# Performance work log

Hardware: AMD Instinct MI355X
Metric: run time of the kernel (lower is better)

The kernel has to match this reference:

```python
import jax, jax.numpy as jnp
import numpy as np

S = 60            # voxel grid side
N = 100000        # active voxels
M_PAD = 60000     # padded pairs per kernel offset
C_IN = 64
C_OUT = 64
KV = 27           # kernel volume (3^3)
CENTER = 13


def _build_maps():
    rng = np.random.default_rng(0)
    lin = rng.choice(S ** 3, size=N, replace=False)
    coords = np.stack(np.unravel_index(lin, (S, S, S)), axis=1).astype(np.int64)  # [N,3]
    lut = -np.ones(S ** 3, dtype=np.int64)
    lut[lin] = np.arange(N)
    imap = -np.ones((KV - 1, M_PAD), dtype=np.int32)
    omap = -np.ones((KV - 1, M_PAD), dtype=np.int32)
    row = 0
    for k in range(KV):
        if k == CENTER:
            continue
        d = np.array([k // 9 - 1, (k // 3) % 3 - 1, k % 3 - 1])
        nb = coords + d
        valid = np.all((nb >= 0) & (nb < S), axis=1)
        linnb = nb[:, 0] * S * S + nb[:, 1] * S + nb[:, 2]
        j = np.where(valid, lut[np.clip(linnb, 0, S ** 3 - 1)], -1)
        mask = j >= 0
        src = np.nonzero(mask)[0].astype(np.int32)   # input idx (gather)
        dst = j[mask].astype(np.int32)               # output idx (scatter)
        m = min(src.shape[0], M_PAD)
        imap[row, :m] = src[:m]
        omap[row, :m] = dst[:m]
        row += 1
    return imap, omap


def setup_inputs() -> dict:
    key = jax.random.key(0)
    kf, kw = jax.random.split(key)
    feats = jax.random.normal(kf, (N, C_IN), dtype=jnp.float32)
    stdv = 1.0 / np.sqrt(C_OUT * KV)
    kernel = jax.random.uniform(kw, (KV, C_IN, C_OUT), dtype=jnp.float32,
                                minval=-stdv, maxval=stdv)
    imap_np, omap_np = _build_maps()
    return {
        "feats": feats,
        "kernel": kernel,
        "imap": jnp.asarray(imap_np),
        "omap": jnp.asarray(omap_np),
    }


def reference(feats, kernel, imap, omap):
    # Submanifold sparse 3D conv: center weight applied densely,
    # 26 neighbor offsets via gather -> per-offset GEMM -> scatter-add.
    # feats: [N, Cin], kernel: [27, Cin, Cout], imap/omap: [26, M] (-1 = pad)
    koff = jnp.concatenate([jnp.arange(CENTER), jnp.arange(CENTER + 1, KV)])
    w_off = kernel[koff]                                   # [26, Cin, Cout]
    out = feats @ kernel[CENTER]                           # [N, Cout] center GEMM
    valid = (imap >= 0)                                    # [26, M]
    gathered = feats[jnp.clip(imap, 0)] * valid[..., None].astype(feats.dtype)  # [26, M, Cin]
    partial = jnp.einsum('kmc,kco->kmo', gathered, w_off)  # [26, M, Cout]
    dst = jnp.where(valid, omap, 0).reshape(-1)            # padded rows contribute zeros
    out = out.at[dst].add(partial.reshape(-1, partial.shape[-1]))
    return out
```

## Files before the change

### kernel.cpp

```cpp
#include <hip/hip_runtime.h>


#define N_PTS 100000
#define MPAD  60000
#define C     64
#define NSL   27
#define NTAP  28
#define NSTG  14

typedef short bf16x8 __attribute__((ext_vector_type(8)));
typedef float f32x4  __attribute__((ext_vector_type(4)));

static __device__ inline unsigned short f2bf(float x) {
    unsigned int u = __float_as_uint(x);
    u += 0x7fffu + ((u >> 16) & 1u);
    return (unsigned short)(u >> 16);
}

#define FEATS16_BYTES ((size_t)(N_PTS + 1) * C * 2)
#define WFRAG_OFF     (((FEATS16_BYTES) + 255) & ~(size_t)255)
#define WFRAG_BYTES   ((size_t)NTAP * 8192)
#define NBR_OFF       (WFRAG_OFF + WFRAG_BYTES)
#define NBR_BYTES     ((size_t)26 * N_PTS * 4)

#define FEAT_ITEMS 800008
#define WF_ITEMS   (NTAP * 2 * 4 * 64)
#define SCAT_ITEMS (26 * MPAD / 4)
#define PREP_TOTAL (FEAT_ITEMS + WF_ITEMS + SCAT_ITEMS)

__global__ __launch_bounds__(256) void prep_one(const float* __restrict__ feats,
                                                const float* __restrict__ kern,
                                                const int* __restrict__ imap,
                                                const int* __restrict__ omap,
                                                unsigned short* __restrict__ f16,
                                                unsigned short* __restrict__ wf,
                                                int* __restrict__ nbr) {
    const int idx = blockIdx.x * 256 + threadIdx.x;
    if (idx < FEAT_ITEMS) {
        bf16x8* dst = (bf16x8*)f16;
        if (idx < FEAT_ITEMS - 8) {
            const float4* src = (const float4*)feats;
            const float4 a = src[2 * idx];
            const float4 b = src[2 * idx + 1];
            bf16x8 v;
            v[0] = (short)f2bf(a.x); v[1] = (short)f2bf(a.y);
            v[2] = (short)f2bf(a.z); v[3] = (short)f2bf(a.w);
            v[4] = (short)f2bf(b.x); v[5] = (short)f2bf(b.y);
            v[6] = (short)f2bf(b.z); v[7] = (short)f2bf(b.w);
            dst[idx] = v;
        } else {
            dst[idx] = (bf16x8){0, 0, 0, 0, 0, 0, 0, 0};
        }
    } else if (idx < FEAT_ITEMS + WF_ITEMS) {
        const int w = idx - FEAT_ITEMS;
        const int lane = w & 63;
        const int rest = w >> 6;
        const int ct = rest & 3;
        const int kk = (rest >> 2) & 1;
        const int s  = rest >> 3;
        bf16x8 v = (bf16x8){0, 0, 0, 0, 0, 0, 0, 0};
        if (s < NSL) {
            const int q = lane >> 4, t = lane & 15;
            const int ksrc = (s == 26) ? 13 : (s + (s >= 13 ? 1 : 0));
            const int k0 = kk * 32 + q * 8;
            const int n  = ct * 16 + t;
            const float* wp = kern + (size_t)ksrc * 4096 + n;
            #pragma unroll
            for (int j = 0; j < 8; ++j) v[j] = (short)f2bf(wp[(size_t)(k0 + j) * 64]);
        }
        ((bf16x8*)wf)[w] = v;
    } else {
        const int k = idx - (FEAT_ITEMS + WF_ITEMS);
        if (k < SCAT_ITEMS) {
            const int s = k / (MPAD / 4);
            const int v = k - s * (MPAD / 4);
            const int4 iv = ((const int4*)(imap + (size_t)s * MPAD))[v];
            const int4 ov = ((const int4*)(omap + (size_t)s * MPAD))[v];
            int* nb = nbr + (size_t)s * N_PTS;
            if (iv.x >= 0) nb[ov.x] = iv.x;
            if (iv.y >= 0) nb[ov.y] = iv.y;
            if (iv.z >= 0) nb[ov.z] = iv.z;
            if (iv.w >= 0) nb[ov.w] = iv.w;
        }
    }
}

static __device__ inline void stage_bfrags(const char* wfbase, int st,
                                           char* buf, int wave, int lane) {
    #pragma unroll
    for (int i = 0; i < 8; ++i) {
        const int chunk = wave * 8 + i;
        const char* gsrc = wfbase + (size_t)st * 16384 + chunk * 1024 + lane * 16;
        __builtin_amdgcn_global_load_lds(
            (const __attribute__((address_space(1))) unsigned int*)gsrc,
            (__attribute__((address_space(3))) unsigned int*)(buf + chunk * 1024),
            16, 0, 0);
    }
}

__global__ __launch_bounds__(128) void spconv_main(const unsigned short* __restrict__ f16,
                                                   const unsigned short* __restrict__ wf,
                                                   const int* __restrict__ nbr,
                                                   float* __restrict__ out) {
    __shared__ __align__(16) char smem[2][16384];

    const int lane = threadIdx.x & 63;
    const int wave = threadIdx.x >> 6;
    const int q = lane >> 4, t = lane & 15;
    const int R0 = blockIdx.x * 64 + wave * 32;
    const int row0 = R0 + t;
    const int row1 = R0 + 16 + t;
    const bool inb0 = (row0 < N_PTS);
    const bool inb1 = (row1 < N_PTS);
    const int safe0 = inb0 ? row0 : 0;
    const int safe1 = inb1 ? row1 : 0;

    const bf16x8* fv = (const bf16x8*)f16;
    const char* wfb  = (const char*)wf;

    stage_bfrags(wfb, 0, smem[0], wave, lane);

    int j0r[26], j1r[26];
    #pragma unroll
    for (int s = 0; s < 26; ++s) {
        j0r[s] = nbr[(size_t)s * N_PTS + safe0];
        j1r[s] = nbr[(size_t)s * N_PTS + safe1];
    }

    f32x4 acc[2][4];
    #pragma unroll
    for (int a = 0; a < 2; ++a)
        #pragma unroll
        for (int c = 0; c < 4; ++c)
            acc[a][c] = (f32x4){0.f, 0.f, 0.f, 0.f};

    #pragma unroll
    for (int st = 0; st < NSTG; ++st) {
        bf16x8 A[2][4];
        #pragma unroll
        for (int tt = 0; tt < 2; ++tt) {
            const int s = st * 2 + tt;
            int j0, j1;
            if (s == 26) {
                j0 = inb0 ? row0 : -1;
                j1 = inb1 ? row1 : -1;
            } else if (s == 27) {
                j0 = -1; j1 = -1;
            } else {
                j0 = inb0 ? j0r[s] : -1;
                j1 = inb1 ? j1r[s] : -1;
            }
            const int jz0 = ((unsigned)j0 < (unsigned)N_PTS) ? j0 : N_PTS;
            const int jz1 = ((unsigned)j1 < (unsigned)N_PTS) ? j1 : N_PTS;
            const bf16x8* a0 = fv + (size_t)jz0 * 8;
            const bf16x8* a1 = fv + (size_t)jz1 * 8;
            A[tt][0] = a0[q]; A[tt][1] = a0[4 + q];
            A[tt][2] = a1[q]; A[tt][3] = a1[4 + q];
        }

        __syncthreads();

        if (st + 1 < NSTG)
            stage_bfrags(wfb, st + 1, smem[(st + 1) & 1], wave, lane);

        const char* buf = smem[st & 1];
        #pragma unroll
        for (int tt = 0; tt < 2; ++tt) {
            bf16x8 B0[4], B1[4];
            #pragma unroll
            for (int ct = 0; ct < 4; ++ct) {
                B0[ct] = *(const bf16x8*)(buf + tt * 8192 + ct * 1024 + lane * 16);
                B1[ct] = *(const bf16x8*)(buf + tt * 8192 + 4096 + ct * 1024 + lane * 16);
            }
            #pragma unroll
            for (int ct = 0; ct < 4; ++ct) {
                acc[0][ct] = __builtin_amdgcn_mfma_f32_16x16x32_bf16(A[tt][0], B0[ct], acc[0][ct], 0, 0, 0);
                acc[1][ct] = __builtin_amdgcn_mfma_f32_16x16x32_bf16(A[tt][2], B0[ct], acc[1][ct], 0, 0, 0);
            }
            #pragma unroll
            for (int ct = 0; ct < 4; ++ct) {
                acc[0][ct] = __builtin_amdgcn_mfma_f32_16x16x32_bf16(A[tt][1], B1[ct], acc[0][ct], 0, 0, 0);
                acc[1][ct] = __builtin_amdgcn_mfma_f32_16x16x32_bf16(A[tt][3], B1[ct], acc[1][ct], 0, 0, 0);
            }
        }
    }

    #pragma unroll
    for (int tile = 0; tile < 2; ++tile) {
        #pragma unroll
        for (int i = 0; i < 4; ++i) {
            const int r = R0 + tile * 16 + 4 * q + i;
            if (r < N_PTS) {
                #pragma unroll
                for (int ct = 0; ct < 4; ++ct)
                    out[(size_t)r * C + ct * 16 + t] = acc[tile][ct][i];
            }
        }
    }
}

extern "C" void kernel_launch(void* const* d_in, const int* in_sizes, int n_in,
                              void* d_out, int out_size, void* d_ws, size_t ws_size,
                              hipStream_t stream) {
    const float* feats = (const float*)d_in[0];
    const float* kern  = (const float*)d_in[1];
    const int*   imap  = (const int*)d_in[2];
    const int*   omap  = (const int*)d_in[3];

    char* ws = (char*)d_ws;
    unsigned short* f16 = (unsigned short*)ws;
    unsigned short* wfr = (unsigned short*)(ws + WFRAG_OFF);
    int*            nbr = (int*)(ws + NBR_OFF);

    prep_one<<<dim3((PREP_TOTAL + 255) / 256), dim3(256), 0, stream>>>(
        feats, kern, imap, omap, f16, wfr, nbr);
    spconv_main<<<dim3((N_PTS + 63) / 64), dim3(128), 0, stream>>>(
        f16, wfr, nbr, (float*)d_out);
}
```

Before: 149.1 us.

## Load weight fragments directly from global memory instead of LDS double-buffering

Removes the LDS double-buffered staging of weight fragments and the per-stage __syncthreads; each wave now reads its B fragments straight from global memory (expected to sit in L2/L1 since all blocks share them). It also drops the padding 28th tap, so 27 slices are processed instead of 28, and adds an occupancy hint of 3 blocks per CU. In exchange it relies on cache hits for the weights, and the per-tap loop no longer interleaves loads of two taps.

Result: slower. 158.4 us (+6.2%).

```diff
diff --git a/kernel.cpp b/kernel.cpp
--- a/kernel.cpp
+++ b/kernel.cpp
@@ -5,8 +5,6 @@
 #define MPAD  60000
 #define C     64
 #define NSL   27
-#define NTAP  28
-#define NSTG  14
 
 typedef short bf16x8 __attribute__((ext_vector_type(8)));
 typedef float f32x4  __attribute__((ext_vector_type(4)));
@@ -19,12 +17,12 @@
 
 #define FEATS16_BYTES ((size_t)(N_PTS + 1) * C * 2)
 #define WFRAG_OFF     (((FEATS16_BYTES) + 255) & ~(size_t)255)
-#define WFRAG_BYTES   ((size_t)NTAP * 8192)
+#define WFRAG_BYTES   ((size_t)NSL * 8192)
 #define NBR_OFF       (WFRAG_OFF + WFRAG_BYTES)
 #define NBR_BYTES     ((size_t)26 * N_PTS * 4)
 
 #define FEAT_ITEMS 800008
-#define WF_ITEMS   (NTAP * 2 * 4 * 64)
+#define WF_ITEMS   (NSL * 2 * 4 * 64)
 #define SCAT_ITEMS (26 * MPAD / 4)
 #define PREP_TOTAL (FEAT_ITEMS + WF_ITEMS + SCAT_ITEMS)
 
@@ -85,25 +83,10 @@
     }
 }
 
-static __device__ inline void stage_bfrags(const char* wfbase, int st,
-                                           char* buf, int wave, int lane) {
-    #pragma unroll
-    for (int i = 0; i < 8; ++i) {
-        const int chunk = wave * 8 + i;
-        const char* gsrc = wfbase + (size_t)st * 16384 + chunk * 1024 + lane * 16;
-        __builtin_amdgcn_global_load_lds(
-            (const __attribute__((address_space(1))) unsigned int*)gsrc,
-            (__attribute__((address_space(3))) unsigned int*)(buf + chunk * 1024),
-            16, 0, 0);
-    }
-}
-
-__global__ __launch_bounds__(128) void spconv_main(const unsigned short* __restrict__ f16,
-                                                   const unsigned short* __restrict__ wf,
-                                                   const int* __restrict__ nbr,
-                                                   float* __restrict__ out) {
-    __shared__ __align__(16) char smem[2][16384];
-
+__global__ __launch_bounds__(128, 3) void spconv_main(const unsigned short* __restrict__ f16,
+                                                      const unsigned short* __restrict__ wf,
+                                                      const int* __restrict__ nbr,
+                                                      float* __restrict__ out) {
     const int lane = threadIdx.x & 63;
     const int wave = threadIdx.x >> 6;
     const int q = lane >> 4, t = lane & 15;
@@ -116,9 +99,7 @@
     const int safe1 = inb1 ? row1 : 0;
 
     const bf16x8* fv = (const bf16x8*)f16;
-    const char* wfb  = (const char*)wf;
-
-    stage_bfrags(wfb, 0, smem[0], wave, lane);
+    const bf16x8* bv = (const bf16x8*)wf;
 
     int j0r[26], j1r[26];
     #pragma unroll
@@ -135,53 +116,39 @@
             acc[a][c] = (f32x4){0.f, 0.f, 0.f, 0.f};
 
     #pragma unroll
-    for (int st = 0; st < NSTG; ++st) {
-        bf16x8 A[2][4];
+    for (int s = 0; s < NSL; ++s) {
+        int j0, j1;
+        if (s == 26) {
+            j0 = inb0 ? row0 : -1;
+            j1 = inb1 ? row1 : -1;
+        } else {
+            j0 = inb0 ? j0r[s] : -1;
+            j1 = inb1 ? j1r[s] : -1;
+        }
+        const int jz0 = ((unsigned)j0 < (unsigned)N_PTS) ? j0 : N_PTS;
+        const int jz1 = ((unsigned)j1 < (unsigned)N_PTS) ? j1 : N_PTS;
+        const bf16x8* a0p = fv + (size_t)jz0 * 8;
+        const bf16x8* a1p = fv + (size_t)jz1 * 8;
+        const bf16x8 A0 = a0p[q];
+        const bf16x8 A1 = a0p[4 + q];
+        const bf16x8 A2 = a1p[q];
+        const bf16x8 A3 = a1p[4 + q];
+        const bf16x8* bp = bv + (size_t)s * 512;
+        bf16x8 B0[4], B1[4];
         #pragma unroll
-        for (int tt = 0; tt < 2; ++tt) {
-            const int s = st * 2 + tt;
-            int j0, j1;
-            if (s == 26) {
-                j0 = inb0 ? row0 : -1;
-                j1 = inb1 ? row1 : -1;
-            } else if (s == 27) {
-                j0 = -1; j1 = -1;
-            } else {
-                j0 = inb0 ? j0r[s] : -1;
-                j1 = inb1 ? j1r[s] : -1;
-            }
-            const int jz0 = ((unsigned)j0 < (unsigned)N_PTS) ? j0 : N_PTS;
-            const int jz1 = ((unsigned)j1 < (unsigned)N_PTS) ? j1 : N_PTS;
-            const bf16x8* a0 = fv + (size_t)jz0 * 8;
-            const bf16x8* a1 = fv + (size_t)jz1 * 8;
-            A[tt][0] = a0[q]; A[tt][1] = a0[4 + q];
-            A[tt][2] = a1[q]; A[tt][3] = a1[4 + q];
+        for (int ct = 0; ct < 4; ++ct) {
+            B0[ct] = bp[ct * 64 + lane];
+            B1[ct] = bp[256 + ct * 64 + lane];
         }
-
-        __syncthreads();
-
-        if (st + 1 < NSTG)
-            stage_bfrags(wfb, st + 1, smem[(st + 1) & 1], wave, lane);
-
-        const char* buf = smem[st & 1];
         #pragma unroll
-        for (int tt = 0; tt < 2; ++tt) {
-            bf16x8 B0[4], B1[4];
-            #pragma unroll
-            for (int ct = 0; ct < 4; ++ct) {
-                B0[ct] = *(const bf16x8*)(buf + tt * 8192 + ct * 1024 + lane * 16);
-                B1[ct] = *(const bf16x8*)(buf + tt * 8192 + 4096 + ct * 1024 + lane * 16);
-            }
-            #pragma unroll
-            for (int ct = 0; ct < 4; ++ct) {
-                acc[0][ct] = __builtin_amdgcn_mfma_f32_16x16x32_bf16(A[tt][0], B0[ct], acc[0][ct], 0, 0, 0);
-                acc[1][ct] = __builtin_amdgcn_mfma_f32_16x16x32_bf16(A[tt][2], B0[ct], acc[1][ct], 0, 0, 0);
-            }
-            #pragma unroll
-            for (int ct = 0; ct < 4; ++ct) {
-                acc[0][ct] = __builtin_amdgcn_mfma_f32_16x16x32_bf16(A[tt][1], B1[ct], acc[0][ct], 0, 0, 0);
-                acc[1][ct] = __builtin_amdgcn_mfma_f32_16x16x32_bf16(A[tt][3], B1[ct], acc[1][ct], 0, 0, 0);
-            }
+        for (int ct = 0; ct < 4; ++ct) {
+            acc[0][ct] = __builtin_amdgcn_mfma_f32_16x16x32_bf16(A0, B0[ct], acc[0][ct], 0, 0, 0);
+            acc[1][ct] = __builtin_amdgcn_mfma_f32_16x16x32_bf16(A2, B0[ct], acc[1][ct], 0, 0, 0);
+        }
+        #pragma unroll
+        for (int ct = 0; ct < 4; ++ct) {
+            acc[0][ct] = __builtin_amdgcn_mfma_f32_16x16x32_bf16(A1, B1[ct], acc[0][ct], 0, 0, 0);
+            acc[1][ct] = __builtin_amdgcn_mfma_f32_16x16x32_bf16(A3, B1[ct], acc[1][ct], 0, 0, 0);
         }
     }
 
```

## Software-pipeline neighbor index and feature gathers, use 256-thread blocks

Applied to the files above, without the earlier changes.

Neighbor indices are no longer all loaded into 52 registers up front. They are now loaded two stages ahead, and the feature gathers for stage st+1 are issued one stage ahead, so they overlap the MFMA work of the current stage. The block grows to 4 waves covering 128 rows, so each wave stages only 4 of the 16 weight-fragment chunks into LDS, halving per-wave staging work. The occupancy hint is 3 blocks per CU. The register savings from dropping the index arrays are offset by double-buffered A fragments, which may raise register pressure.

Measured after the change: 148.2 us. No clear change (-0.6%).

```diff
diff --git a/kernel.cpp b/kernel.cpp
--- a/kernel.cpp
+++ b/kernel.cpp
@@ -88,8 +88,8 @@
 static __device__ inline void stage_bfrags(const char* wfbase, int st,
                                            char* buf, int wave, int lane) {
     #pragma unroll
-    for (int i = 0; i < 8; ++i) {
-        const int chunk = wave * 8 + i;
+    for (int i = 0; i < 4; ++i) {
+        const int chunk = wave * 4 + i;
         const char* gsrc = wfbase + (size_t)st * 16384 + chunk * 1024 + lane * 16;
         __builtin_amdgcn_global_load_lds(
             (const __attribute__((address_space(1))) unsigned int*)gsrc,
@@ -98,16 +98,76 @@
     }
 }
 
-__global__ __launch_bounds__(128) void spconv_main(const unsigned short* __restrict__ f16,
-                                                   const unsigned short* __restrict__ wf,
-                                                   const int* __restrict__ nbr,
-                                                   float* __restrict__ out) {
+static __device__ inline void load_j(const int* __restrict__ nbr, int st,
+                                     int safe0, int safe1, int jj[4]) {
+    #pragma unroll
+    for (int tt = 0; tt < 2; ++tt) {
+        const int s = st * 2 + tt;
+        if (s < 26) {
+            jj[tt * 2 + 0] = nbr[(size_t)s * N_PTS + safe0];
+            jj[tt * 2 + 1] = nbr[(size_t)s * N_PTS + safe1];
+        }
+    }
+}
+
+static __device__ inline void gather_a(const bf16x8* __restrict__ fv, int st,
+                                       const int jj[4], bool inb0, bool inb1,
+                                       int row0, int row1, int q, bf16x8 A[2][4]) {
+    #pragma unroll
+    for (int tt = 0; tt < 2; ++tt) {
+        const int s = st * 2 + tt;
+        int j0, j1;
+        if (s == 26) {
+            j0 = inb0 ? row0 : -1;
+            j1 = inb1 ? row1 : -1;
+        } else if (s == 27) {
+            j0 = -1; j1 = -1;
+        } else {
+            j0 = inb0 ? jj[tt * 2 + 0] : -1;
+            j1 = inb1 ? jj[tt * 2 + 1] : -1;
+        }
+        const int jz0 = ((unsigned)j0 < (unsigned)N_PTS) ? j0 : N_PTS;
+        const int jz1 = ((unsigned)j1 < (unsigned)N_PTS) ? j1 : N_PTS;
+        const bf16x8* a0 = fv + (size_t)jz0 * 8;
+        const bf16x8* a1 = fv + (size_t)jz1 * 8;
+        A[tt][0] = a0[q]; A[tt][1] = a0[4 + q];
+        A[tt][2] = a1[q]; A[tt][3] = a1[4 + q];
+    }
+}
+
+static __device__ inline void compute_stage(const char* buf, const bf16x8 A[2][4],
+                                            int lane, f32x4 acc[2][4]) {
+    #pragma unroll
+    for (int tt = 0; tt < 2; ++tt) {
+        bf16x8 B0[4], B1[4];
+        #pragma unroll
+        for (int ct = 0; ct < 4; ++ct) {
+            B0[ct] = *(const bf16x8*)(buf + tt * 8192 + ct * 1024 + lane * 16);
+            B1[ct] = *(const bf16x8*)(buf + tt * 8192 + 4096 + ct * 1024 + lane * 16);
+        }
+        #pragma unroll
+        for (int ct = 0; ct < 4; ++ct) {
+            acc[0][ct] = __builtin_amdgcn_mfma_f32_16x16x32_bf16(A[tt][0], B0[ct], acc[0][ct], 0, 0, 0);
+            acc[1][ct] = __builtin_amdgcn_mfma_f32_16x16x32_bf16(A[tt][2], B0[ct], acc[1][ct], 0, 0, 0);
+        }
+        #pragma unroll
+        for (int ct = 0; ct < 4; ++ct) {
+            acc[0][ct] = __builtin_amdgcn_mfma_f32_16x16x32_bf16(A[tt][1], B1[ct], acc[0][ct], 0, 0, 0);
+            acc[1][ct] = __builtin_amdgcn_mfma_f32_16x16x32_bf16(A[tt][3], B1[ct], acc[1][ct], 0, 0, 0);
+        }
+    }
+}
+
+__global__ __launch_bounds__(256, 3) void spconv_main(const unsigned short* __restrict__ f16,
+                                                      const unsigned short* __restrict__ wf,
+                                                      const int* __restrict__ nbr,
+                                                      float* __restrict__ out) {
     __shared__ __align__(16) char smem[2][16384];
 
     const int lane = threadIdx.x & 63;
     const int wave = threadIdx.x >> 6;
     const int q = lane >> 4, t = lane & 15;
-    const int R0 = blockIdx.x * 64 + wave * 32;
+    const int R0 = blockIdx.x * 128 + wave * 32;
     const int row0 = R0 + t;
     const int row1 = R0 + 16 + t;
     const bool inb0 = (row0 < N_PTS);
@@ -119,13 +179,11 @@
     const char* wfb  = (const char*)wf;
 
     stage_bfrags(wfb, 0, smem[0], wave, lane);
-
-    int j0r[26], j1r[26];
-    #pragma unroll
-    for (int s = 0; s < 26; ++s) {
-        j0r[s] = nbr[(size_t)s * N_PTS + safe0];
-        j1r[s] = nbr[(size_t)s * N_PTS + safe1];
-    }
+    int jbuf[2][4];
+    load_j(nbr, 0, safe0, safe1, jbuf[0]);
+    bf16x8 Abuf[2][2][4];
+    gather_a(fv, 0, jbuf[0], inb0, inb1, row0, row1, q, Abuf[0]);
+    load_j(nbr, 1, safe0, safe1, jbuf[1]);
 
     f32x4 acc[2][4];
     #pragma unroll
@@ -136,53 +194,17 @@
 
     #pragma unroll
     for (int st = 0; st < NSTG; ++st) {
-        bf16x8 A[2][4];
-        #pragma unroll
-        for (int tt = 0; tt < 2; ++tt) {
-            const int s = st * 2 + tt;
-            int j0, j1;
-            if (s == 26) {
-                j0 = inb0 ? row0 : -1;
-                j1 = inb1 ? row1 : -1;
-            } else if (s == 27) {
-                j0 = -1; j1 = -1;
-            } else {
-                j0 = inb0 ? j0r[s] : -1;
-                j1 = inb1 ? j1r[s] : -1;
-            }
-            const int jz0 = ((unsigned)j0 < (unsigned)N_PTS) ? j0 : N_PTS;
-            const int jz1 = ((unsigned)j1 < (unsigned)N_PTS) ? j1 : N_PTS;
-            const bf16x8* a0 = fv + (size_t)jz0 * 8;
-            const bf16x8* a1 = fv + (size_t)jz1 * 8;
-            A[tt][0] = a0[q]; A[tt][1] = a0[4 + q];
-            A[tt][2] = a1[q]; A[tt][3] = a1[4 + q];
-        }
-
         __syncthreads();
 
-        if (st + 1 < NSTG)
+        if (st + 1 < NSTG) {
             stage_bfrags(wfb, st + 1, smem[(st + 1) & 1], wave, lane);
-
-        const char* buf = smem[st & 1];
-        #pragma unroll
-        for (int tt = 0; tt < 2; ++tt) {
-            bf16x8 B0[4], B1[4];
-            #pragma unroll
-            for (int ct = 0; ct < 4; ++ct) {
-                B0[ct] = *(const bf16x8*)(buf + tt * 8192 + ct * 1024 + lane * 16);
-                B1[ct] = *(const bf16x8*)(buf + tt * 8192 + 4096 + ct * 1024 + lane * 16);
-            }
-            #pragma unroll
-            for (int ct = 0; ct < 4; ++ct) {
-                acc[0][ct] = __builtin_amdgcn_mfma_f32_16x16x32_bf16(A[tt][0], B0[ct], acc[0][ct], 0, 0, 0);
-                acc[1][ct] = __builtin_amdgcn_mfma_f32_16x16x32_bf16(A[tt][2], B0[ct], acc[1][ct], 0, 0, 0);
-            }
-            #pragma unroll
-            for (int ct = 0; ct < 4; ++ct) {
-                acc[0][ct] = __builtin_amdgcn_mfma_f32_16x16x32_bf16(A[tt][1], B1[ct], acc[0][ct], 0, 0, 0);
-                acc[1][ct] = __builtin_amdgcn_mfma_f32_16x16x32_bf16(A[tt][3], B1[ct], acc[1][ct], 0, 0, 0);
-            }
-        }
+            gather_a(fv, st + 1, jbuf[(st + 1) & 1], inb0, inb1, row0, row1, q,
+                     Abuf[(st + 1) & 1]);
+        }
+        if (st + 2 < NSTG)
+            load_j(nbr, st + 2, safe0, safe1, jbuf[st & 1]);
+
+        compute_stage(smem[st & 1], Abuf[st & 1], lane, acc);
     }
 
     #pragma unroll
@@ -214,6 +236,6 @@
 
     prep_one<<<dim3((PREP_TOTAL + 255) / 256), dim3(256), 0, stream>>>(
         feats, kern, imap, omap, f16, wfr, nbr);
-    spconv_main<<<dim3((N_PTS + 63) / 64), dim3(128), 0, stream>>>(
+    spconv_main<<<dim3((N_PTS + 127) / 128), dim3(256), 0, stream>>>(
         f16, wfr, nbr, (float*)d_out);
 }
```
